# Kernel optimization log

Measured on AMD Instinct MI355X. Metric: run time of the kernel, lower is better.

## Reference

```python
import jax, jax.numpy as jnp
import numpy as np

H = W = 56      # image resolution
WS = 7          # window size
SS = 3          # shift size
NH = 8          # num heads
E = 256         # embed dim
HD = E // NH    # head dim (qkv Linear operates per-head on HD)
NW = (H // WS) * (W // WS)  # 64 windows
WD = WS * WS                # 49 tokens per window


def _rel_pos_index():
    coords = np.stack(np.meshgrid(np.arange(WS), np.arange(WS), indexing='ij'))  # (2,WS,WS)
    cf = coords.reshape(2, -1)
    rel = (cf[:, :, None] - cf[:, None, :]).transpose(1, 2, 0)  # (WD,WD,2)
    rel[..., 0] += WS - 1
    rel[..., 1] += WS - 1
    rel[..., 0] *= 2 * WS - 1
    return rel.sum(-1)  # (WD,WD) ints in [0, (2WS-1)^2)


def _attn_mask():
    # Swin shifted-window attention mask: -100 where tokens come from different regions.
    m = np.zeros((H, W))
    slices = (slice(0, -WS), slice(-WS, -SS), slice(-SS, None))
    cnt = 0
    for hs in slices:
        for ws in slices:
            m[hs, ws] = cnt
            cnt += 1
    mw = m.reshape(H // WS, WS, W // WS, WS).transpose(0, 2, 1, 3).reshape(NW, WD)
    diff = mw[:, None, :] - mw[:, :, None]  # (NW,WD,WD)
    return np.where(diff != 0, -100.0, 0.0).astype(np.float32)


def setup_inputs() -> dict:
    key = jax.random.key(0)
    ks = jax.random.split(key, 6)
    return {
        'x': jax.random.normal(ks[0], (32, H * W, E), jnp.float32),
        'qkv_w': jax.random.normal(ks[1], (HD, 3 * HD), jnp.float32) * 0.05,
        'qkv_b': jax.random.normal(ks[2], (3 * HD,), jnp.float32) * 0.05,
        'proj_w': jax.random.normal(ks[3], (E, E), jnp.float32) * 0.05,
        'proj_b': jax.random.normal(ks[4], (E,), jnp.float32) * 0.05,
        'rpb_table': jax.random.normal(ks[5], ((2 * WS - 1) ** 2, NH), jnp.float32) * 0.02,
    }


def reference(x, qkv_w, qkv_b, proj_w, proj_b, rpb_table):
    B = x.shape[0]
    rpi = _rel_pos_index()
    bias = rpb_table[rpi.reshape(-1)].reshape(WD, WD, NH).transpose(2, 0, 1)  # (NH,WD,WD)
    mask = jnp.asarray(_attn_mask())  # (NW,WD,WD)

    xs = x.reshape(B, H, W, E)
    xs = jnp.roll(xs, (-SS, -SS), axis=(1, 2))  # cyclic shift (equals cycle_shift)
    # window partition -> (B,NW,WD,E)
    xw = xs.reshape(B, H // WS, WS, W // WS, WS, E).transpose(0, 1, 3, 2, 4, 5).reshape(B, NW, WD, E)
    # split heads -> (B,NW,NH,WD,HD)
    xh = xw.reshape(B, NW, WD, NH, HD).transpose(0, 1, 3, 2, 4)
    qkv = xh @ qkv_w + qkv_b  # per-head shared qkv projection (as in original)
    q, k, v = jnp.split(qkv, 3, axis=-1)
    scores = jnp.einsum('bwhqd,bwhkd->bwhqk', q, k) / np.sqrt(HD).astype(np.float32)
    scores = scores + bias + mask[None, :, None]  # (B,NW,NH,WD,WD)
    attn = jax.nn.softmax(scores, axis=-1)
    o = jnp.einsum('bwhqk,bwhkd->bwhqd', attn, v)
    # merge heads and reverse window partition
    o = o.transpose(0, 1, 3, 2, 4).reshape(B, NW, WD, E)
    o = o.reshape(B, H // WS, W // WS, WS, WS, E).transpose(0, 1, 3, 2, 4, 5).reshape(B, H, W, E)
    o = jnp.roll(o, (SS, SS), axis=(1, 2)).reshape(B, H * W, E)  # reverse cyclic shift
    return o @ proj_w + proj_b
```

## Files before the change

kernel.cpp:

```cpp
#include <hip/hip_runtime.h>
#include <hip/hip_bf16.h>

#define WSZ 7
#define WD  49
#define NH  8
#define NWIN 64
#define HH  56
#define SS  3
#define TOK 3136
#define EMB 256

typedef __attribute__((ext_vector_type(8))) short bf16x8;
typedef __attribute__((ext_vector_type(8))) unsigned short u16x8;
typedef __attribute__((ext_vector_type(4))) float f32x4;

#define OFF_WT   0
#define OFF_POS  7680
#define OFF_PW   7936
#define PW_SZ    14848
#define PW_K     5120
#define PW_VT    10240
#define LDS_TOTAL (OFF_PW + 4*PW_SZ)
#define SO_STRIDE 264

__device__ __forceinline__ unsigned short f2bf(float f) {
    union { float f; unsigned u; } v; v.f = f;
    return (unsigned short)((v.u + 0x7FFFu + ((v.u >> 16) & 1u)) >> 16);
}
__device__ __forceinline__ unsigned long long pack4(float a, float b, float c, float d) {
    return (unsigned long long)f2bf(a) | ((unsigned long long)f2bf(b) << 16)
         | ((unsigned long long)f2bf(c) << 32) | ((unsigned long long)f2bf(d) << 48);
}

__global__ __launch_bounds__(256, 2) void fused_kernel(
    const float* __restrict__ x, const float* __restrict__ qkv_w,
    const float* __restrict__ qkv_b, const unsigned short* __restrict__ Wt,
    const float* __restrict__ proj_b, const float* __restrict__ tbl,
    float* __restrict__ out)
{
    extern __shared__ char smem[];
    unsigned short* sWT = (unsigned short*)(smem + OFF_WT);
    int* sPOS = (int*)(smem + OFF_POS);

    const int tid = threadIdx.x;
    const int w = blockIdx.x & 63, b = blockIdx.x >> 6;
    const int wi = w >> 3, wj = w & 7;
    const int cls = (((wi == 7) ? 1 : 0) << 1) | ((wj == 7) ? 1 : 0);

    if (tid < 64) {
        int ti = tid / 7, tj = tid - (tid / 7) * 7;
        int sh = wi * WSZ + ti, sw = wj * WSZ + tj;
        sPOS[tid] = ((sh + SS) % HH) * HH + ((sw + SS) % HH);
    }
    for (int i = tid; i < 32 * 96; i += 256) {
        int c = i / 96, j = i - c * 96;
        sWT[j * 40 + c] = f2bf(qkv_w[i]);
    }
    __syncthreads();

    const int wave = tid >> 6, lane = tid & 63;
    const int cl = lane & 15, quad = lane >> 4;
    unsigned short* sQ  = (unsigned short*)(smem + OFF_PW + wave * PW_SZ);
    unsigned short* sK  = sQ + PW_K / 2;
    unsigned short* sVT = sQ + PW_VT / 2;
    unsigned short* sP  = sQ;

    const float* xrow[4];
    #pragma unroll
    for (int mt = 0; mt < 4; ++mt)
        xrow[mt] = x + ((size_t)b * TOK + sPOS[mt * 16 + cl]) * EMB + quad * 8;

    const float qscale = 0.17677669529663687f;
    f32x4 otr[2][2][4];

    #pragma unroll
    for (int hi = 0; hi < 2; ++hi) {
        const int h = wave * 2 + hi;
        bf16x8 xa[4];
        #pragma unroll
        for (int mt = 0; mt < 4; ++mt) {
            const float* p = xrow[mt] + h * 32;
            float4 v0 = *(const float4*)p, v1 = *(const float4*)(p + 4);
            union { bf16x8 v; unsigned long long q[2]; } u;
            u.q[0] = pack4(v0.x, v0.y, v0.z, v0.w);
            u.q[1] = pack4(v1.x, v1.y, v1.z, v1.w);
            xa[mt] = u.v;
        }
        #pragma unroll
        for (int mt = 0; mt < 4; ++mt) {
            bf16x8 wa = *(const bf16x8*)(&sWT[(mt * 16 + cl) * 40 + quad * 8]);
            float4 bq = *(const float4*)(qkv_b + mt * 16 + quad * 4);
            #pragma unroll
            for (int nt = 0; nt < 4; ++nt) {
                f32x4 c = {bq.x, bq.y, bq.z, bq.w};
                c = __builtin_amdgcn_mfma_f32_16x16x32_bf16(wa, xa[nt], c, 0, 0, 0);
                int tok = nt * 16 + cl;
                if (mt < 2) {
                    int col0 = mt * 16 + quad * 4;
                    *(unsigned long long*)(&sQ[tok * 40 + col0]) =
                        pack4(c[0] * qscale, c[1] * qscale, c[2] * qscale, c[3] * qscale);
                } else {
                    int col0 = (mt - 2) * 16 + quad * 4;
                    *(unsigned long long*)(&sK[tok * 40 + col0]) =
                        pack4(c[0], c[1], c[2], c[3]);
                }
            }
        }
        #pragma unroll
        for (int nt = 4; nt < 6; ++nt) {
            bf16x8 wv = *(const bf16x8*)(&sWT[(nt * 16 + cl) * 40 + quad * 8]);
            float bb = qkv_b[nt * 16 + cl];
            #pragma unroll
            for (int mt = 0; mt < 4; ++mt) {
                f32x4 c = {bb, bb, bb, bb};
                c = __builtin_amdgcn_mfma_f32_16x16x32_bf16(xa[mt], wv, c, 0, 0, 0);
                int hd = nt * 16 + cl - 64;
                *(unsigned long long*)(&sVT[hd * 72 + mt * 16 + quad * 4]) =
                    pack4(c[0], c[1], c[2], c[3]);
            }
        }
        bf16x8 kb[4], qa[4];
        #pragma unroll
        for (int mt = 0; mt < 4; ++mt) kb[mt] = *(const bf16x8*)(&sK[(mt * 16 + cl) * 40 + quad * 8]);
        #pragma unroll
        for (int nt = 0; nt < 4; ++nt) qa[nt] = *(const bf16x8*)(&sQ[(nt * 16 + cl) * 40 + quad * 8]);
        const float* tb = tbl + ((size_t)(cls * 8 + h) * 16) * 256 + lane * 4;
        f32x4 sc[4][4];
        #pragma unroll
        for (int mt = 0; mt < 4; ++mt)
            #pragma unroll
            for (int nt = 0; nt < 4; ++nt) {
                f32x4 c = *(const f32x4*)(tb + (mt * 4 + nt) * 256);
                sc[mt][nt] = __builtin_amdgcn_mfma_f32_16x16x32_bf16(kb[mt], qa[nt], c, 0, 0, 0);
            }
        #pragma unroll
        for (int nt = 0; nt < 4; ++nt) {
            float e[4][4];
            float sm = 0.f;
            #pragma unroll
            for (int mt = 0; mt < 4; ++mt)
                #pragma unroll
                for (int r = 0; r < 4; ++r) {
                    float v = __expf(sc[mt][nt][r]);
                    e[mt][r] = v; sm += v;
                }
            sm += __shfl_xor(sm, 16);
            sm += __shfl_xor(sm, 32);
            float inv = 1.f / sm;
            int qt = nt * 16 + cl;
            #pragma unroll
            for (int mt = 0; mt < 4; ++mt)
                *(unsigned long long*)(&sP[qt * 72 + mt * 16 + quad * 4]) =
                    pack4(e[mt][0] * inv, e[mt][1] * inv, e[mt][2] * inv, e[mt][3] * inv);
        }
        #pragma unroll
        for (int mv = 0; mv < 2; ++mv)
            #pragma unroll
            for (int nt = 0; nt < 4; ++nt) otr[hi][mv][nt] = (f32x4){0.f, 0.f, 0.f, 0.f};
        #pragma unroll
        for (int ks = 0; ks < 2; ++ks) {
            bf16x8 va[2], pb[4];
            #pragma unroll
            for (int mv = 0; mv < 2; ++mv)
                va[mv] = *(const bf16x8*)(&sVT[(mv * 16 + cl) * 72 + ks * 32 + quad * 8]);
            #pragma unroll
            for (int nt = 0; nt < 4; ++nt)
                pb[nt] = *(const bf16x8*)(&sP[(nt * 16 + cl) * 72 + ks * 32 + quad * 8]);
            #pragma unroll
            for (int mv = 0; mv < 2; ++mv)
                #pragma unroll
                for (int nt = 0; nt < 4; ++nt)
                    otr[hi][mv][nt] = __builtin_amdgcn_mfma_f32_16x16x32_bf16(va[mv], pb[nt], otr[hi][mv][nt], 0, 0, 0);
        }
    }

    __syncthreads();
    unsigned short* sO = (unsigned short*)(smem + OFF_PW);
    #pragma unroll
    for (int hi = 0; hi < 2; ++hi) {
        const int h = wave * 2 + hi;
        #pragma unroll
        for (int mv = 0; mv < 2; ++mv)
            #pragma unroll
            for (int nt = 0; nt < 4; ++nt) {
                int qt = nt * 16 + cl;
                f32x4 o = otr[hi][mv][nt];
                *(unsigned long long*)(&sO[qt * SO_STRIDE + h * 32 + mv * 16 + quad * 4]) =
                    pack4(o[0], o[1], o[2], o[3]);
            }
    }
    __syncthreads();

    const int n0 = wave * 64;
    f32x4 acc[4][4];
    #pragma unroll
    for (int mt = 0; mt < 4; ++mt)
        #pragma unroll
        for (int tt = 0; tt < 4; ++tt) acc[mt][tt] = (f32x4){0.f, 0.f, 0.f, 0.f};
    #pragma unroll
    for (int ks = 0; ks < 8; ++ks) {
        bf16x8 wa[4], ob[4];
        #pragma unroll
        for (int mt = 0; mt < 4; ++mt)
            wa[mt] = *(const bf16x8*)(Wt + (size_t)(n0 + mt * 16 + cl) * 256 + ks * 32 + quad * 8);
        #pragma unroll
        for (int tt = 0; tt < 4; ++tt)
            ob[tt] = *(const bf16x8*)(&sO[(tt * 16 + cl) * SO_STRIDE + ks * 32 + quad * 8]);
        #pragma unroll
        for (int mt = 0; mt < 4; ++mt)
            #pragma unroll
            for (int tt = 0; tt < 4; ++tt)
                acc[mt][tt] = __builtin_amdgcn_mfma_f32_16x16x32_bf16(wa[mt], ob[tt], acc[mt][tt], 0, 0, 0);
    }
    #pragma unroll
    for (int mt = 0; mt < 4; ++mt) {
        float4 bq = *(const float4*)(proj_b + n0 + mt * 16 + quad * 4);
        #pragma unroll
        for (int tt = 0; tt < 4; ++tt) {
            int tok = tt * 16 + cl;
            if (tok < WD) {
                f32x4 v = acc[mt][tt];
                v[0] += bq.x; v[1] += bq.y; v[2] += bq.z; v[3] += bq.w;
                float* dst = out + ((size_t)b * TOK + sPOS[tok]) * EMB + n0 + mt * 16 + quad * 4;
                *(f32x4*)dst = v;
            }
        }
    }
}

__global__ __launch_bounds__(256) void cvt_kernel(
    const float* __restrict__ W, unsigned short* __restrict__ Wt)
{
    int i = blockIdx.x * 256 + threadIdx.x;
    int k = i >> 8, n = i & 255;
    Wt[n * 256 + k] = f2bf(W[i]);
}

__global__ __launch_bounds__(256) void tbl_kernel(
    const float* __restrict__ rpb, float* __restrict__ tbl)
{
    int idx = blockIdx.x * 256 + threadIdx.x;
    int r = idx & 3;
    int lane = (idx >> 2) & 63;
    int cl = lane & 15, quad = lane >> 4;
    int tile = (idx >> 8) & 15;
    int mt = tile >> 2, nt = tile & 3;
    int h = (idx >> 12) & 7;
    int cls = (idx >> 15) & 3;
    int ci = cls >> 1, cj = cls & 1;

    int ktok = mt * 16 + quad * 4 + r;
    int qtok = nt * 16 + cl;

    float v;
    if (ktok >= WD) v = -1e30f;
    else if (qtok >= WD) v = 0.f;
    else {
        int qi = qtok / 7, qj = qtok - qi * 7;
        int ki = ktok / 7, kj = ktok - ki * 7;
        v = rpb[((qi - ki + 6) * 13 + (qj - kj + 6)) * NH + h];
        int qreg = (ci ? (qi < 4 ? 1 : 2) : 0) * 3 + (cj ? (qj < 4 ? 1 : 2) : 0);
        int kreg = (ci ? (ki < 4 ? 1 : 2) : 0) * 3 + (cj ? (kj < 4 ? 1 : 2) : 0);
        if (qreg != kreg) v -= 100.f;
    }
    tbl[idx] = v;
}

extern "C" void kernel_launch(void* const* d_in, const int* in_sizes, int n_in,
                              void* d_out, int out_size, void* d_ws, size_t ws_size,
                              hipStream_t stream) {
    const float* x      = (const float*)d_in[0];
    const float* qkv_w  = (const float*)d_in[1];
    const float* qkv_b  = (const float*)d_in[2];
    const float* proj_w = (const float*)d_in[3];
    const float* proj_b = (const float*)d_in[4];
    const float* rpb    = (const float*)d_in[5];
    float* out = (float*)d_out;

    const int B = in_sizes[0] / (TOK * EMB);

    unsigned short* Wt = (unsigned short*)d_ws;
    float* tbl = (float*)((char*)d_ws + 131072);

    (void)hipFuncSetAttribute(reinterpret_cast<const void*>(&fused_kernel),
                              hipFuncAttributeMaxDynamicSharedMemorySize, LDS_TOTAL);
    cvt_kernel<<<256, 256, 0, stream>>>(proj_w, Wt);
    tbl_kernel<<<512, 256, 0, stream>>>(rpb, tbl);
    fused_kernel<<<B * NWIN, 256, LDS_TOTAL, stream>>>(x, qkv_w, qkv_b, Wt, proj_b, tbl, out);
}
```

Before: 257.3 us.

## Shrink LDS with swizzled per-wave tiles, keep qkv weights and positions in registers

```diff
diff --git a/kernel.cpp b/kernel.cpp
--- a/kernel.cpp
+++ b/kernel.cpp
@@ -11,16 +11,12 @@
 #define EMB 256
 
 typedef __attribute__((ext_vector_type(8))) short bf16x8;
-typedef __attribute__((ext_vector_type(8))) unsigned short u16x8;
 typedef __attribute__((ext_vector_type(4))) float f32x4;
 
-#define OFF_WT   0
-#define OFF_POS  7680
-#define OFF_PW   7936
-#define PW_SZ    14848
-#define PW_K     5120
-#define PW_VT    10240
-#define LDS_TOTAL (OFF_PW + 4*PW_SZ)
+#define SWZ(row, col) ((col) ^ (((row) & 7) << 3))
+#define PW_SH   6144
+#define VT_SH   4096
+#define LDS_TOTAL 49152
 #define SO_STRIDE 264
 
 __device__ __forceinline__ unsigned short f2bf(float f) {
@@ -32,43 +28,73 @@
          | ((unsigned long long)f2bf(c) << 32) | ((unsigned long long)f2bf(d) << 48);
 }
 
-__global__ __launch_bounds__(256, 2) void fused_kernel(
+__global__ __launch_bounds__(256, 3) void fused_kernel(
     const float* __restrict__ x, const float* __restrict__ qkv_w,
-    const float* __restrict__ qkv_b, const unsigned short* __restrict__ Wt,
+    const float* __restrict__ qkv_b, const unsigned short* __restrict__ pWt,
     const float* __restrict__ proj_b, const float* __restrict__ tbl,
     float* __restrict__ out)
 {
     extern __shared__ char smem[];
-    unsigned short* sWT = (unsigned short*)(smem + OFF_WT);
-    int* sPOS = (int*)(smem + OFF_POS);
 
     const int tid = threadIdx.x;
     const int w = blockIdx.x & 63, b = blockIdx.x >> 6;
     const int wi = w >> 3, wj = w & 7;
     const int cls = (((wi == 7) ? 1 : 0) << 1) | ((wj == 7) ? 1 : 0);
-
-    if (tid < 64) {
-        int ti = tid / 7, tj = tid - (tid / 7) * 7;
-        int sh = wi * WSZ + ti, sw = wj * WSZ + tj;
-        sPOS[tid] = ((sh + SS) % HH) * HH + ((sw + SS) % HH);
-    }
-    for (int i = tid; i < 32 * 96; i += 256) {
-        int c = i / 96, j = i - c * 96;
-        sWT[j * 40 + c] = f2bf(qkv_w[i]);
-    }
-    __syncthreads();
-
     const int wave = tid >> 6, lane = tid & 63;
     const int cl = lane & 15, quad = lane >> 4;
-    unsigned short* sQ  = (unsigned short*)(smem + OFF_PW + wave * PW_SZ);
-    unsigned short* sK  = sQ + PW_K / 2;
-    unsigned short* sVT = sQ + PW_VT / 2;
-    unsigned short* sP  = sQ;
-
-    const float* xrow[4];
-    #pragma unroll
-    for (int mt = 0; mt < 4; ++mt)
-        xrow[mt] = x + ((size_t)b * TOK + sPOS[mt * 16 + cl]) * EMB + quad * 8;
+
+    int pos4[4];
+    #pragma unroll
+    for (int mt = 0; mt < 4; ++mt) {
+        int tok = mt * 16 + cl;
+        int ti = (tok * 37) >> 8;
+        int tj = tok - ti * 7;
+        int r = wi * WSZ + ti + SS; if (r >= HH) r -= HH;
+        int c = wj * WSZ + tj + SS; if (c >= HH) c -= HH;
+        pos4[mt] = r * HH + c;
+    }
+
+    bf16x8 wQK[4]; float4 bQK[4];
+    #pragma unroll
+    for (int mt = 0; mt < 4; ++mt) {
+        const float* wp = qkv_w + quad * 8 * 96 + (mt * 16 + cl);
+        union { bf16x8 v; unsigned long long q[2]; } u;
+        u.q[0] = pack4(wp[0],   wp[96],  wp[192], wp[288]);
+        u.q[1] = pack4(wp[384], wp[480], wp[576], wp[672]);
+        wQK[mt] = u.v;
+        bQK[mt] = *(const float4*)(qkv_b + mt * 16 + quad * 4);
+    }
+    bf16x8 wV[2]; float bV[2];
+    #pragma unroll
+    for (int i = 0; i < 2; ++i) {
+        const float* wp = qkv_w + quad * 8 * 96 + (64 + i * 16 + cl);
+        union { bf16x8 v; unsigned long long q[2]; } u;
+        u.q[0] = pack4(wp[0],   wp[96],  wp[192], wp[288]);
+        u.q[1] = pack4(wp[384], wp[480], wp[576], wp[672]);
+        wV[i] = u.v;
+        bV[i] = qkv_b[64 + i * 16 + cl];
+    }
+
+    bf16x8 xa2[2][4];
+    #pragma unroll
+    for (int mt = 0; mt < 4; ++mt) {
+        const float* p = x + ((size_t)b * TOK + pos4[mt]) * EMB + quad * 8 + wave * 64;
+        float4 v0 = *(const float4*)p;
+        float4 v1 = *(const float4*)(p + 4);
+        float4 v2 = *(const float4*)(p + 32);
+        float4 v3 = *(const float4*)(p + 36);
+        union { bf16x8 v; unsigned long long q[2]; } u0, u1;
+        u0.q[0] = pack4(v0.x, v0.y, v0.z, v0.w);
+        u0.q[1] = pack4(v1.x, v1.y, v1.z, v1.w);
+        u1.q[0] = pack4(v2.x, v2.y, v2.z, v2.w);
+        u1.q[1] = pack4(v3.x, v3.y, v3.z, v3.w);
+        xa2[0][mt] = u0.v;
+        xa2[1][mt] = u1.v;
+    }
+
+    unsigned short* sT  = (unsigned short*)smem + wave * PW_SH;
+    unsigned short* sVT = sT + VT_SH;
+    unsigned short* sP  = sT;
 
     const float qscale = 0.17677669529663687f;
     f32x4 otr[2][2][4];
@@ -76,54 +102,46 @@
     #pragma unroll
     for (int hi = 0; hi < 2; ++hi) {
         const int h = wave * 2 + hi;
-        bf16x8 xa[4];
         #pragma unroll
         for (int mt = 0; mt < 4; ++mt) {
-            const float* p = xrow[mt] + h * 32;
-            float4 v0 = *(const float4*)p, v1 = *(const float4*)(p + 4);
-            union { bf16x8 v; unsigned long long q[2]; } u;
-            u.q[0] = pack4(v0.x, v0.y, v0.z, v0.w);
-            u.q[1] = pack4(v1.x, v1.y, v1.z, v1.w);
-            xa[mt] = u.v;
-        }
-        #pragma unroll
-        for (int mt = 0; mt < 4; ++mt) {
-            bf16x8 wa = *(const bf16x8*)(&sWT[(mt * 16 + cl) * 40 + quad * 8]);
-            float4 bq = *(const float4*)(qkv_b + mt * 16 + quad * 4);
             #pragma unroll
             for (int nt = 0; nt < 4; ++nt) {
-                f32x4 c = {bq.x, bq.y, bq.z, bq.w};
-                c = __builtin_amdgcn_mfma_f32_16x16x32_bf16(wa, xa[nt], c, 0, 0, 0);
+                f32x4 c = {bQK[mt].x, bQK[mt].y, bQK[mt].z, bQK[mt].w};
+                c = __builtin_amdgcn_mfma_f32_16x16x32_bf16(wQK[mt], xa2[hi][nt], c, 0, 0, 0);
                 int tok = nt * 16 + cl;
                 if (mt < 2) {
                     int col0 = mt * 16 + quad * 4;
-                    *(unsigned long long*)(&sQ[tok * 40 + col0]) =
+                    *(unsigned long long*)(&sT[tok * 64 + SWZ(tok, col0)]) =
                         pack4(c[0] * qscale, c[1] * qscale, c[2] * qscale, c[3] * qscale);
                 } else {
-                    int col0 = (mt - 2) * 16 + quad * 4;
-                    *(unsigned long long*)(&sK[tok * 40 + col0]) =
+                    int col0 = 32 + (mt - 2) * 16 + quad * 4;
+                    *(unsigned long long*)(&sT[tok * 64 + SWZ(tok, col0)]) =
                         pack4(c[0], c[1], c[2], c[3]);
                 }
             }
         }
         #pragma unroll
-        for (int nt = 4; nt < 6; ++nt) {
-            bf16x8 wv = *(const bf16x8*)(&sWT[(nt * 16 + cl) * 40 + quad * 8]);
-            float bb = qkv_b[nt * 16 + cl];
+        for (int i = 0; i < 2; ++i) {
             #pragma unroll
             for (int mt = 0; mt < 4; ++mt) {
-                f32x4 c = {bb, bb, bb, bb};
-                c = __builtin_amdgcn_mfma_f32_16x16x32_bf16(xa[mt], wv, c, 0, 0, 0);
-                int hd = nt * 16 + cl - 64;
-                *(unsigned long long*)(&sVT[hd * 72 + mt * 16 + quad * 4]) =
+                f32x4 c = {bV[i], bV[i], bV[i], bV[i]};
+                c = __builtin_amdgcn_mfma_f32_16x16x32_bf16(xa2[hi][mt], wV[i], c, 0, 0, 0);
+                int hd = i * 16 + cl;
+                *(unsigned long long*)(&sVT[hd * 64 + SWZ(hd, mt * 16 + quad * 4)]) =
                     pack4(c[0], c[1], c[2], c[3]);
             }
         }
         bf16x8 kb[4], qa[4];
         #pragma unroll
-        for (int mt = 0; mt < 4; ++mt) kb[mt] = *(const bf16x8*)(&sK[(mt * 16 + cl) * 40 + quad * 8]);
-        #pragma unroll
-        for (int nt = 0; nt < 4; ++nt) qa[nt] = *(const bf16x8*)(&sQ[(nt * 16 + cl) * 40 + quad * 8]);
+        for (int mt = 0; mt < 4; ++mt) {
+            int rk = mt * 16 + cl;
+            kb[mt] = *(const bf16x8*)(&sT[rk * 64 + SWZ(rk, 32 + quad * 8)]);
+        }
+        #pragma unroll
+        for (int nt = 0; nt < 4; ++nt) {
+            int rq = nt * 16 + cl;
+            qa[nt] = *(const bf16x8*)(&sT[rq * 64 + SWZ(rq, quad * 8)]);
+        }
         const float* tb = tbl + ((size_t)(cls * 8 + h) * 16) * 256 + lane * 4;
         f32x4 sc[4][4];
         #pragma unroll
@@ -150,7 +168,7 @@
             int qt = nt * 16 + cl;
             #pragma unroll
             for (int mt = 0; mt < 4; ++mt)
-                *(unsigned long long*)(&sP[qt * 72 + mt * 16 + quad * 4]) =
+                *(unsigned long long*)(&sP[qt * 64 + SWZ(qt, mt * 16 + quad * 4)]) =
                     pack4(e[mt][0] * inv, e[mt][1] * inv, e[mt][2] * inv, e[mt][3] * inv);
         }
         #pragma unroll
@@ -161,11 +179,15 @@
         for (int ks = 0; ks < 2; ++ks) {
             bf16x8 va[2], pb[4];
             #pragma unroll
-            for (int mv = 0; mv < 2; ++mv)
-                va[mv] = *(const bf16x8*)(&sVT[(mv * 16 + cl) * 72 + ks * 32 + quad * 8]);
-            #pragma unroll
-            for (int nt = 0; nt < 4; ++nt)
-                pb[nt] = *(const bf16x8*)(&sP[(nt * 16 + cl) * 72 + ks * 32 + quad * 8]);
+            for (int mv = 0; mv < 2; ++mv) {
+                int rv = mv * 16 + cl;
+                va[mv] = *(const bf16x8*)(&sVT[rv * 64 + SWZ(rv, ks * 32 + quad * 8)]);
+            }
+            #pragma unroll
+            for (int nt = 0; nt < 4; ++nt) {
+                int rp = nt * 16 + cl;
+                pb[nt] = *(const bf16x8*)(&sP[rp * 64 + SWZ(rp, ks * 32 + quad * 8)]);
+            }
             #pragma unroll
             for (int mv = 0; mv < 2; ++mv)
                 #pragma unroll
@@ -175,7 +197,7 @@
     }
 
     __syncthreads();
-    unsigned short* sO = (unsigned short*)(smem + OFF_PW);
+    unsigned short* sO = (unsigned short*)smem;
     #pragma unroll
     for (int hi = 0; hi < 2; ++hi) {
         const int h = wave * 2 + hi;
@@ -202,7 +224,7 @@
         bf16x8 wa[4], ob[4];
         #pragma unroll
         for (int mt = 0; mt < 4; ++mt)
-            wa[mt] = *(const bf16x8*)(Wt + (size_t)(n0 + mt * 16 + cl) * 256 + ks * 32 + quad * 8);
+            wa[mt] = *(const bf16x8*)(pWt + (size_t)(n0 + mt * 16 + cl) * 256 + ks * 32 + quad * 8);
         #pragma unroll
         for (int tt = 0; tt < 4; ++tt)
             ob[tt] = *(const bf16x8*)(&sO[(tt * 16 + cl) * SO_STRIDE + ks * 32 + quad * 8]);
@@ -221,7 +243,7 @@
             if (tok < WD) {
                 f32x4 v = acc[mt][tt];
                 v[0] += bq.x; v[1] += bq.y; v[2] += bq.z; v[3] += bq.w;
-                float* dst = out + ((size_t)b * TOK + sPOS[tok]) * EMB + n0 + mt * 16 + quad * 4;
+                float* dst = out + ((size_t)b * TOK + pos4[tt]) * EMB + n0 + mt * 16 + quad * 4;
                 *(f32x4*)dst = v;
             }
         }
@@ -279,12 +301,12 @@
 
     const int B = in_sizes[0] / (TOK * EMB);
 
-    unsigned short* Wt = (unsigned short*)d_ws;
+    unsigned short* pWt = (unsigned short*)d_ws;
     float* tbl = (float*)((char*)d_ws + 131072);
 
     (void)hipFuncSetAttribute(reinterpret_cast<const void*>(&fused_kernel),
                               hipFuncAttributeMaxDynamicSharedMemorySize, LDS_TOTAL);
-    cvt_kernel<<<256, 256, 0, stream>>>(proj_w, Wt);
+    cvt_kernel<<<256, 256, 0, stream>>>(proj_w, pWt);
     tbl_kernel<<<512, 256, 0, stream>>>(rpb, tbl);
-    fused_kernel<<<B * NWIN, 256, LDS_TOTAL, stream>>>(x, qkv_w, qkv_b, Wt, proj_b, tbl, out);
-}
+    fused_kernel<<<B * NWIN, 256, LDS_TOTAL, stream>>>(x, qkv_w, qkv_b, pWt, proj_b, tbl, out);
+}
```

Result: slower. 281.6 us (+9.5%).
